# Kernel optimization log

Hardware: AMD Instinct MI355X
Metric: run time of the kernel (lower is better)

Reference implementation:

```python
import jax, jax.numpy as jnp
import numpy as np


def conv1x1(x, W, b):
    # x: [B,C,H,W], W: [O,C], b: [O]
    return jnp.einsum('bchw,oc->bohw', x, W) + b[None, :, None, None]


def setup_inputs() -> dict:
    key = jax.random.key(0)
    ks = jax.random.split(key, 16)
    B, C, H, W = 4, 256, 64, 64
    C4 = C // 4
    s = lambda fan_in: 1.0 / np.sqrt(fan_in)
    inp = {
        'last_frame': jax.random.normal(ks[0], (B, C, H, W), jnp.float32),
        'current_frame': jax.random.normal(ks[1], (B, C, H, W), jnp.float32),
        'future_frame': jax.random.normal(ks[2], (B, C, H, W), jnp.float32),
        'Wqk': jax.random.normal(ks[3], (C4, C), jnp.float32) * s(C),
        'bqk': jnp.zeros((C4,), jnp.float32),
        'Wkl': jax.random.normal(ks[4], (C4, C), jnp.float32) * s(C),
        'bkl': jnp.zeros((C4,), jnp.float32),
        'Wkf': jax.random.normal(ks[5], (C4, C), jnp.float32) * s(C),
        'bkf': jnp.zeros((C4,), jnp.float32),
        'Wv': jax.random.normal(ks[6], (C4, C), jnp.float32) * s(C),
        'bv': jnp.zeros((C4,), jnp.float32),
        'Wfire': jax.random.normal(ks[7], (C, C // 2), jnp.float32) * s(C // 2),
        'bfire': jnp.zeros((C,), jnp.float32),
        'bn_gamma': jnp.ones((C,), jnp.float32),
        'bn_beta': jnp.zeros((C,), jnp.float32),
        'bn_mean': jnp.zeros((C,), jnp.float32),
        'bn_var': jnp.ones((C,), jnp.float32),
    }
    return inp


def reference(last_frame, current_frame, future_frame,
              Wqk, bqk, Wkl, bkl, Wkf, bkf, Wv, bv,
              Wfire, bfire, bn_gamma, bn_beta, bn_mean, bn_var):
    B, C, H, W = current_frame.shape
    C4 = C // 4
    HW = H * W
    eps = 1e-5

    q = conv1x1(current_frame, Wqk, bqk).reshape(B, C4, HW)       # [B,C4,HW]
    kl = conv1x1(last_frame, Wkl, bkl).reshape(B, C4, HW)          # [B,C4,HW]
    kf = conv1x1(future_frame, Wkf, bkf).reshape(B, C4, HW)        # [B,C4,HW]
    v = conv1x1(current_frame, Wv, bv).reshape(B, C4, HW)          # [B,C4,HW]

    # affinity: [B, HW(query), HW(key)], softmax over key axis
    aff_l = jax.nn.softmax(jnp.einsum('bcq,bck->bqk', q, kl), axis=-1)
    aff_f = jax.nn.softmax(jnp.einsum('bcq,bck->bqk', q, kf), axis=-1)

    # out = V @ A^T : out[b,c,q] = sum_k v[b,c,k] * aff[b,q,k]
    out_l = jnp.einsum('bck,bqk->bcq', v, aff_l).reshape(B, C4, H, W)
    out_f = jnp.einsum('bck,bqk->bcq', v, aff_f).reshape(B, C4, H, W)

    fused = jnp.concatenate([out_l, out_f], axis=1)                 # [B,C/2,H,W]
    fired = conv1x1(fused, Wfire, bfire)                            # [B,C,H,W]
    # BatchNorm (inference form with running stats)
    inv = bn_gamma / jnp.sqrt(bn_var + eps)
    fired = fired * inv[None, :, None, None] + (bn_beta - bn_mean * inv)[None, :, None, None]
    return jax.nn.relu(current_frame + fired)
```

## Files before the change

### kernel.cpp

```cpp
#include <hip/hip_runtime.h>
#include <math.h>
#include <stdint.h>

#define HWN 4096
#define CIN 256
#define CQ 64
#define LOG2E 1.44269504f
#define C2OFF 56.0f

typedef __attribute__((ext_vector_type(8))) _Float16 f16x8;
typedef __attribute__((ext_vector_type(4))) _Float16 f16x4;
typedef __attribute__((ext_vector_type(8))) short    bf16x8;
typedef __attribute__((ext_vector_type(4))) short    bf16x4;
typedef __attribute__((ext_vector_type(4))) float    f32x4;

__device__ __forceinline__ short f2bf(float f) {
  union { float f; uint32_t u; } c; c.f = f;
  uint32_t r = (c.u + 0x7FFFu + ((c.u >> 16) & 1u)) >> 16;
  return (short)(uint16_t)r;
}

__device__ __forceinline__ void stage16(const void* g, void* l) {
  __builtin_amdgcn_global_load_lds(
      (const __attribute__((address_space(1))) uint32_t*)g,
      (__attribute__((address_space(3))) uint32_t*)l, 16, 0, 0);
}

__global__ __launch_bounds__(256) void prep_kernel(
    const float* __restrict__ Wqk, const float* __restrict__ Wkl,
    const float* __restrict__ Wkf, const float* __restrict__ Wv,
    const float* __restrict__ Wfire, const float* __restrict__ bfire,
    const float* __restrict__ gamma, const float* __restrict__ beta,
    const float* __restrict__ mean,  const float* __restrict__ var,
    _Float16* __restrict__ wqk_h, _Float16* __restrict__ wkl_h,
    _Float16* __restrict__ wkf_h, _Float16* __restrict__ wv_h,
    _Float16* __restrict__ wf_h, float* __restrict__ scale, float* __restrict__ shift) {
  int gid = blockIdx.x * 256 + threadIdx.x;
  if (gid < CQ * CIN) {
    wqk_h[gid] = (_Float16)(Wqk[gid] * LOG2E);
    wkl_h[gid] = (_Float16)Wkl[gid];
    wkf_h[gid] = (_Float16)Wkf[gid];
    wv_h[gid]  = (_Float16)Wv[gid];
  }
  if (gid < CIN * 128) wf_h[gid] = (_Float16)Wfire[gid];
  if (gid < CIN) {
    float inv = gamma[gid] / sqrtf(var[gid] + 1e-5f);
    scale[gid] = inv;
    shift[gid] = (bfire[gid] - mean[gid]) * inv + beta[gid];
  }
}

__global__ __launch_bounds__(256, 3) void proj_kernel(
    const float* __restrict__ cur, const float* __restrict__ last, const float* __restrict__ fut,
    const _Float16* __restrict__ wqk, const float* __restrict__ bqk,
    const _Float16* __restrict__ wkl, const float* __restrict__ bkl,
    const _Float16* __restrict__ wkf, const float* __restrict__ bkf,
    const _Float16* __restrict__ wv,  const float* __restrict__ bv,
    _Float16* __restrict__ q_out, _Float16* __restrict__ kl_out,
    _Float16* __restrict__ kf_out, short* __restrict__ v_out) {
  const int tid  = threadIdx.x;
  const int w    = tid >> 6;
  const int lane = tid & 63;
  const int quad = lane >> 4;
  const int l15  = lane & 15;
  const int pass = blockIdx.x >> 8;
  const int bb   = blockIdx.x & 255;
  const int b    = bb >> 6;
  const int hwt  = (bb & 63) << 6;
  const int hw   = hwt + w * 16 + l15;

  __shared__ __align__(16) _Float16 Tl[4][16][72];

  const float* X = (pass == 0) ? cur : ((pass == 1) ? last : fut);
  const float* xp = X + (size_t)b * CIN * HWN + hw;

  float xb[8][8];
#pragma unroll
  for (int c0 = 0; c0 < 8; ++c0)
#pragma unroll
    for (int j = 0; j < 8; ++j)
      xb[c0][j] = xp[(size_t)(c0 * 32 + quad * 8 + j) * HWN];

  if (pass == 0) {
    f32x4 aq[4] = {}; f32x4 av[4] = {};
#pragma unroll
    for (int k0 = 0; k0 < 8; ++k0) {
      f16x8 bh;
#pragma unroll
      for (int j = 0; j < 8; ++j) bh[j] = (_Float16)xb[k0][j];
#pragma unroll
      for (int mt = 0; mt < 4; ++mt) {
        f16x8 wa = *(const f16x8*)(wqk + (mt * 16 + l15) * CIN + k0 * 32 + quad * 8);
        aq[mt] = __builtin_amdgcn_mfma_f32_16x16x32_f16(wa, bh, aq[mt], 0, 0, 0);
        f16x8 wb = *(const f16x8*)(wv + (mt * 16 + l15) * CIN + k0 * 32 + quad * 8);
        av[mt] = __builtin_amdgcn_mfma_f32_16x16x32_f16(wb, bh, av[mt], 0, 0, 0);
      }
    }
#pragma unroll
    for (int mt = 0; mt < 4; ++mt)
#pragma unroll
      for (int r = 0; r < 4; ++r) {
        int oc = mt * 16 + quad * 4 + r;
        q_out[((size_t)b * CQ + oc) * HWN + hw] = (_Float16)(aq[mt][r] + bqk[oc] * LOG2E);
        v_out[((size_t)b * CQ + oc) * HWN + hw] = f2bf(av[mt][r] + bv[oc]);
      }
  } else {
    const _Float16* W = (pass == 1) ? wkl : wkf;
    const float* BI = (pass == 1) ? bkl : bkf;
    _Float16* OUT = (pass == 1) ? kl_out : kf_out;
    f32x4 a[4] = {};
#pragma unroll
    for (int k0 = 0; k0 < 8; ++k0) {
      f16x8 bh;
#pragma unroll
      for (int j = 0; j < 8; ++j) bh[j] = (_Float16)xb[k0][j];
#pragma unroll
      for (int mt = 0; mt < 4; ++mt) {
        f16x8 wa = *(const f16x8*)(W + (mt * 16 + l15) * CIN + k0 * 32 + quad * 8);
        a[mt] = __builtin_amdgcn_mfma_f32_16x16x32_f16(wa, bh, a[mt], 0, 0, 0);
      }
    }
#pragma unroll
    for (int mt = 0; mt < 4; ++mt) {
      f16x4 pw;
#pragma unroll
      for (int r = 0; r < 4; ++r)
        pw[r] = (_Float16)(a[mt][r] + BI[mt * 16 + quad * 4 + r]);
      *(f16x4*)&Tl[w][l15][mt * 16 + quad * 4] = pw;
    }
#pragma unroll
    for (int kk = 0; kk < 2; ++kk) {
      f16x8 row = *(const f16x8*)&Tl[w][l15][kk * 32 + quad * 8];
      *(f16x8*)(OUT + ((size_t)b * HWN + hw) * CQ + kk * 32 + quad * 8) = row;
    }
  }
}

__global__ __launch_bounds__(256, 2) void attn_kernel(
    const _Float16* __restrict__ qbuf, const _Float16* __restrict__ klbuf,
    const _Float16* __restrict__ kfbuf, const short* __restrict__ vbuf,
    _Float16* __restrict__ fused) {
  const int tid  = threadIdx.x;
  const int w    = tid >> 6;
  const int lane = tid & 63;
  const int quad = lane >> 4;
  const int l15  = lane & 15;
  const int bx   = blockIdx.x;
  const int pair = bx & 1;
  const int b    = (bx >> 1) & 3;
  const int qt   = (bx >> 3) << 6;

  const _Float16* K  = (pair ? kfbuf : klbuf) + (size_t)b * HWN * CQ;
  const short*    Vg = vbuf + (size_t)b * CQ * HWN;

  __shared__ __align__(16) _Float16 Kt[2][64][64];
  __shared__ __align__(16) short    Vt[2][64][64];
  __shared__ __align__(16) short    Pl[4][16][72];

  const int qbase = qt + w * 16;
  f16x8 qfrag[2];
#pragma unroll
  for (int kk = 0; kk < 2; ++kk)
#pragma unroll
    for (int j = 0; j < 8; ++j)
      qfrag[kk][j] = qbuf[(b * CQ + kk * 32 + quad * 8 + j) * HWN + qbase + l15];

  f32x4 Oacc[4] = {};
  float psum = 0.f;

  const int swz = (lane & 7) ^ ((lane >> 3) & 7);
  const int rswz = l15 & 7;

  auto stageK = [&](int buf, int t) {
#pragma unroll
    for (int r = 0; r < 2; ++r)
      stage16(K + (size_t)(t * 64 + w * 16 + r * 8 + (lane >> 3)) * CQ + swz * 8,
              &Kt[buf][w * 16 + r * 8][0]);
  };
  auto stageV = [&](int buf, int t) {
#pragma unroll
    for (int r = 0; r < 2; ++r)
      stage16(Vg + (size_t)(w * 16 + r * 8 + (lane >> 3)) * HWN + t * 64 + swz * 8,
              &Vt[buf][w * 16 + r * 8][0]);
  };

  auto body = [&](int buf) {
    f16x8 kf[4][2];
#pragma unroll
    for (int nt = 0; nt < 4; ++nt)
#pragma unroll
      for (int kk = 0; kk < 2; ++kk)
        kf[nt][kk] = *(const f16x8*)&Kt[buf][nt * 16 + l15][((kk * 4 + quad) ^ rswz) * 8];
    bf16x8 vf[4][2];
#pragma unroll
    for (int ct = 0; ct < 4; ++ct)
#pragma unroll
      for (int kk = 0; kk < 2; ++kk)
        vf[ct][kk] = *(const bf16x8*)&Vt[buf][ct * 16 + l15][((kk * 4 + quad) ^ rswz) * 8];
    f32x4 ST[4] = {};
#pragma unroll
    for (int nt = 0; nt < 4; ++nt)
#pragma unroll
      for (int kk = 0; kk < 2; ++kk)
        ST[nt] = __builtin_amdgcn_mfma_f32_16x16x32_f16(kf[nt][kk], qfrag[kk], ST[nt], 0, 0, 0);
#pragma unroll
    for (int nt = 0; nt < 4; ++nt) {
      bf16x4 pw;
#pragma unroll
      for (int r = 0; r < 4; ++r) {
        float p = __builtin_amdgcn_exp2f(ST[nt][r] - C2OFF);
        uint32_t u = __float_as_uint(p) & 0xffff0000u;
        psum += __uint_as_float(u);
        pw[r] = (short)(u >> 16);
      }
      *(bf16x4*)&Pl[w][l15][nt * 16 + quad * 4] = pw;
    }
#pragma unroll
    for (int kk = 0; kk < 2; ++kk) {
      bf16x8 pf = *(const bf16x8*)&Pl[w][l15][kk * 32 + quad * 8];
#pragma unroll
      for (int ct = 0; ct < 4; ++ct)
        Oacc[ct] = __builtin_amdgcn_mfma_f32_16x16x32_bf16(pf, vf[ct][kk], Oacc[ct], 0, 0, 0);
    }
  };

  stageK(0, 0); stageV(0, 0);
  __syncthreads();
#pragma unroll 1
  for (int tt = 0; tt < 64; tt += 2) {
    stageK(1, tt + 1); stageV(1, tt + 1);
    body(0);
    __syncthreads();
    if (tt + 2 < 64) { stageK(0, tt + 2); stageV(0, tt + 2); }
    body(1);
    __syncthreads();
  }

  psum += __shfl_xor(psum, 16);
  psum += __shfl_xor(psum, 32);

#pragma unroll
  for (int r = 0; r < 4; ++r) {
    float lt = __shfl(psum, quad * 4 + r);
    float invl = __builtin_amdgcn_rcpf(lt);
    int qi = qbase + quad * 4 + r;
#pragma unroll
    for (int ct = 0; ct < 4; ++ct)
      fused[((size_t)b * HWN + qi) * 128 + pair * 64 + ct * 16 + l15] =
          (_Float16)(Oacc[ct][r] * invl);
  }
}

__global__ __launch_bounds__(256) void fire_kernel(
    const _Float16* __restrict__ fused, const _Float16* __restrict__ wf,
    const float* __restrict__ scale, const float* __restrict__ shift,
    const float* __restrict__ cur, float* __restrict__ out) {
  const int tid  = threadIdx.x;
  const int w    = tid >> 6;
  const int lane = tid & 63;
  const int quad = lane >> 4;
  const int l15  = lane & 15;
  const int g    = blockIdx.x & 3;
  const int bb   = blockIdx.x >> 2;
  const int b    = bb >> 6;
  const int hwt  = (bb & 63) << 6;
  const int hwb  = hwt + w * 16;

  f16x8 bfr[4];
#pragma unroll
  for (int k0 = 0; k0 < 4; ++k0)
    bfr[k0] = *(const f16x8*)(fused + ((size_t)b * HWN + hwb + l15) * 128 + k0 * 32 + quad * 8);

  float curv[4][4];
#pragma unroll
  for (int mt = 0; mt < 4; ++mt)
#pragma unroll
    for (int r = 0; r < 4; ++r)
      curv[mt][r] = cur[((size_t)b * CIN + g * 64 + mt * 16 + quad * 4 + r) * HWN + hwb + l15];

  f32x4 acc[4] = {};
#pragma unroll
  for (int k0 = 0; k0 < 4; ++k0)
#pragma unroll
    for (int mt = 0; mt < 4; ++mt) {
      f16x8 af = *(const f16x8*)(wf + (g * 64 + mt * 16 + l15) * 128 + k0 * 32 + quad * 8);
      acc[mt] = __builtin_amdgcn_mfma_f32_16x16x32_f16(af, bfr[k0], acc[mt], 0, 0, 0);
    }

#pragma unroll
  for (int mt = 0; mt < 4; ++mt)
#pragma unroll
    for (int r = 0; r < 4; ++r) {
      int oc = g * 64 + mt * 16 + quad * 4 + r;
      size_t idx = ((size_t)b * CIN + oc) * HWN + hwb + l15;
      float y = curv[mt][r] + acc[mt][r] * scale[oc] + shift[oc];
      out[idx] = fmaxf(y, 0.f);
    }
}

extern "C" void kernel_launch(void* const* d_in, const int* in_sizes, int n_in,
                              void* d_out, int out_size, void* d_ws, size_t ws_size,
                              hipStream_t stream) {
  const float* last  = (const float*)d_in[0];
  const float* cur   = (const float*)d_in[1];
  const float* fut   = (const float*)d_in[2];
  const float* Wqk   = (const float*)d_in[3];
  const float* bqk   = (const float*)d_in[4];
  const float* Wkl   = (const float*)d_in[5];
  const float* bkl   = (const float*)d_in[6];
  const float* Wkf   = (const float*)d_in[7];
  const float* bkf   = (const float*)d_in[8];
  const float* Wv    = (const float*)d_in[9];
  const float* bv    = (const float*)d_in[10];
  const float* Wfire = (const float*)d_in[11];
  const float* bfire = (const float*)d_in[12];
  const float* gamma = (const float*)d_in[13];
  const float* beta  = (const float*)d_in[14];
  const float* mean  = (const float*)d_in[15];
  const float* var   = (const float*)d_in[16];

  char* ws = (char*)d_ws;
  _Float16* qb     = (_Float16*)(ws);
  _Float16* klb    = (_Float16*)(ws + (2u << 20));
  _Float16* kfb    = (_Float16*)(ws + (4u << 20));
  short*    vb     = (short*)   (ws + (6u << 20));
  _Float16* fusedb = (_Float16*)(ws + (8u << 20));
  char* wsm = ws + (12u << 20);
  _Float16* wqk_h = (_Float16*)(wsm);
  _Float16* wkl_h = (_Float16*)(wsm + (32u << 10));
  _Float16* wkf_h = (_Float16*)(wsm + (64u << 10));
  _Float16* wv_h  = (_Float16*)(wsm + (96u << 10));
  _Float16* wf_h  = (_Float16*)(wsm + (128u << 10));
  float*    scale = (float*)   (wsm + (192u << 10));
  float*    shift = (float*)   (wsm + (193u << 10));
  float*    out   = (float*)d_out;

  prep_kernel<<<128, 256, 0, stream>>>(Wqk, Wkl, Wkf, Wv, Wfire, bfire,
                                       gamma, beta, mean, var,
                                       wqk_h, wkl_h, wkf_h, wv_h, wf_h, scale, shift);
  proj_kernel<<<768, 256, 0, stream>>>(cur, last, fut, wqk_h, bqk, wkl_h, bkl,
                                       wkf_h, bkf, wv_h, bv, qb, klb, kfb, vb);
  attn_kernel<<<512, 256, 0, stream>>>(qb, klb, kfb, vb, fusedb);
  fire_kernel<<<1024, 256, 0, stream>>>(fusedb, wf_h, scale, shift, cur, out);
}
```

Before: 203.9 us.

## Split key range across wave pairs, read V from global, remap blocks per XCD

The attention kernel now splits its waves into two key halves. Each wave handles 32 queries instead of 16, which reuses each staged K tile across two query groups. The two halves' partial outputs and row sums are combined through shared memory at the end. V fragments are now loaded directly from global memory instead of being staged in LDS, only K is double-buffered, block indices are remapped so each XCD gets contiguous work, and MFMA sections get raised wave priority. This aims to cut LDS traffic and per-query K staging and to improve L2 locality, at the cost of more registers, uncoalesced direct V loads and an extra reduction step.

```diff
diff --git a/kernel.cpp b/kernel.cpp
--- a/kernel.cpp
+++ b/kernel.cpp
@@ -145,109 +145,149 @@
   const int lane = tid & 63;
   const int quad = lane >> 4;
   const int l15  = lane & 15;
-  const int bx   = blockIdx.x;
-  const int pair = bx & 1;
-  const int b    = (bx >> 1) & 3;
-  const int qt   = (bx >> 3) << 6;
+
+  const int xcd  = blockIdx.x & 7;
+  const int L    = xcd * 64 + (blockIdx.x >> 3);
+  const int qt   = (L & 63) << 6;
+  const int pair = (L >> 6) & 1;
+  const int b    = L >> 7;
+
+  const int kh = w >> 1;
+  const int wq = w & 1;
 
   const _Float16* K  = (pair ? kfbuf : klbuf) + (size_t)b * HWN * CQ;
   const short*    Vg = vbuf + (size_t)b * CQ * HWN;
 
-  __shared__ __align__(16) _Float16 Kt[2][64][64];
-  __shared__ __align__(16) short    Vt[2][64][64];
-  __shared__ __align__(16) short    Pl[4][16][72];
-
-  const int qbase = qt + w * 16;
-  f16x8 qfrag[2];
-#pragma unroll
-  for (int kk = 0; kk < 2; ++kk)
-#pragma unroll
-    for (int j = 0; j < 8; ++j)
-      qfrag[kk][j] = qbuf[(b * CQ + kk * 32 + quad * 8 + j) * HWN + qbase + l15];
-
-  f32x4 Oacc[4] = {};
-  float psum = 0.f;
-
-  const int swz = (lane & 7) ^ ((lane >> 3) & 7);
+  __shared__ __align__(16) _Float16 Kt[2][2][64][64];
+  __shared__ __align__(16) short    Pl[4][32][72];
+
+  const int qbase = qt + wq * 32;
+  f16x8 qfrag[2][2];
+#pragma unroll
+  for (int qg = 0; qg < 2; ++qg)
+#pragma unroll
+    for (int kk = 0; kk < 2; ++kk)
+#pragma unroll
+      for (int j = 0; j < 8; ++j)
+        qfrag[qg][kk][j] = qbuf[(b * CQ + kk * 32 + quad * 8 + j) * HWN +
+                                qbase + qg * 16 + l15];
+
+  f32x4 Oacc[2][4] = {};
+  float psum[2] = {0.f, 0.f};
+
+  const int swz  = (lane & 7) ^ ((lane >> 3) & 7);
   const int rswz = l15 & 7;
 
+  const _Float16* ksrc =
+      K + ((size_t)(kh * 32) * 64 + wq * 32 + (lane >> 3)) * CQ + swz * 8;
+  const short* vsrc = Vg + (size_t)l15 * HWN + kh * 2048 + quad * 8;
+
   auto stageK = [&](int buf, int t) {
 #pragma unroll
-    for (int r = 0; r < 2; ++r)
-      stage16(K + (size_t)(t * 64 + w * 16 + r * 8 + (lane >> 3)) * CQ + swz * 8,
-              &Kt[buf][w * 16 + r * 8][0]);
+    for (int r = 0; r < 4; ++r)
+      stage16(ksrc + ((size_t)t * 64 + r * 8) * CQ,
+              &Kt[buf][kh][wq * 32 + r * 8][0]);
   };
-  auto stageV = [&](int buf, int t) {
-#pragma unroll
-    for (int r = 0; r < 2; ++r)
-      stage16(Vg + (size_t)(w * 16 + r * 8 + (lane >> 3)) * HWN + t * 64 + swz * 8,
-              &Vt[buf][w * 16 + r * 8][0]);
+
+  auto body = [&](int buf, int t) {
+    bf16x8 vf[4][2];
+#pragma unroll
+    for (int ct = 0; ct < 4; ++ct)
+#pragma unroll
+      for (int kk = 0; kk < 2; ++kk)
+        vf[ct][kk] = *(const bf16x8*)(vsrc + (size_t)ct * 16 * HWN + t * 64 + kk * 32);
+    f16x8 kf[4][2];
+#pragma unroll
+    for (int nt = 0; nt < 4; ++nt)
+#pragma unroll
+      for (int kk = 0; kk < 2; ++kk)
+        kf[nt][kk] = *(const f16x8*)&Kt[buf][kh][nt * 16 + l15][((kk * 4 + quad) ^ rswz) * 8];
+#pragma unroll
+    for (int qg = 0; qg < 2; ++qg) {
+      f32x4 ST[4] = {};
+      __builtin_amdgcn_s_setprio(1);
+#pragma unroll
+      for (int nt = 0; nt < 4; ++nt)
+#pragma unroll
+        for (int kk = 0; kk < 2; ++kk)
+          ST[nt] = __builtin_amdgcn_mfma_f32_16x16x32_f16(kf[nt][kk], qfrag[qg][kk],
+                                                          ST[nt], 0, 0, 0);
+      __builtin_amdgcn_s_setprio(0);
+#pragma unroll
+      for (int nt = 0; nt < 4; ++nt) {
+        bf16x4 pw;
+#pragma unroll
+        for (int r = 0; r < 4; ++r) {
+          float p = __builtin_amdgcn_exp2f(ST[nt][r] - C2OFF);
+          uint32_t u = __float_as_uint(p) & 0xffff0000u;
+          psum[qg] += __uint_as_float(u);
+          pw[r] = (short)(u >> 16);
+        }
+        *(bf16x4*)&Pl[w][qg * 16 + l15][nt * 16 + quad * 4] = pw;
+      }
+#pragma unroll
+      for (int kk = 0; kk < 2; ++kk) {
+        bf16x8 pf = *(const bf16x8*)&Pl[w][qg * 16 + l15][kk * 32 + quad * 8];
+        __builtin_amdgcn_s_setprio(1);
+#pragma unroll
+        for (int ct = 0; ct < 4; ++ct)
+          Oacc[qg][ct] = __builtin_amdgcn_mfma_f32_16x16x32_bf16(pf, vf[ct][kk],
+                                                                 Oacc[qg][ct], 0, 0, 0);
+        __builtin_amdgcn_s_setprio(0);
+      }
+    }
   };
 
-  auto body = [&](int buf) {
-    f16x8 kf[4][2];
-#pragma unroll
-    for (int nt = 0; nt < 4; ++nt)
-#pragma unroll
-      for (int kk = 0; kk < 2; ++kk)
-        kf[nt][kk] = *(const f16x8*)&Kt[buf][nt * 16 + l15][((kk * 4 + quad) ^ rswz) * 8];
-    bf16x8 vf[4][2];
-#pragma unroll
-    for (int ct = 0; ct < 4; ++ct)
-#pragma unroll
-      for (int kk = 0; kk < 2; ++kk)
-        vf[ct][kk] = *(const bf16x8*)&Vt[buf][ct * 16 + l15][((kk * 4 + quad) ^ rswz) * 8];
-    f32x4 ST[4] = {};
-#pragma unroll
-    for (int nt = 0; nt < 4; ++nt)
-#pragma unroll
-      for (int kk = 0; kk < 2; ++kk)
-        ST[nt] = __builtin_amdgcn_mfma_f32_16x16x32_f16(kf[nt][kk], qfrag[kk], ST[nt], 0, 0, 0);
-#pragma unroll
-    for (int nt = 0; nt < 4; ++nt) {
-      bf16x4 pw;
-#pragma unroll
-      for (int r = 0; r < 4; ++r) {
-        float p = __builtin_amdgcn_exp2f(ST[nt][r] - C2OFF);
-        uint32_t u = __float_as_uint(p) & 0xffff0000u;
-        psum += __uint_as_float(u);
-        pw[r] = (short)(u >> 16);
-      }
-      *(bf16x4*)&Pl[w][l15][nt * 16 + quad * 4] = pw;
-    }
-#pragma unroll
-    for (int kk = 0; kk < 2; ++kk) {
-      bf16x8 pf = *(const bf16x8*)&Pl[w][l15][kk * 32 + quad * 8];
-#pragma unroll
-      for (int ct = 0; ct < 4; ++ct)
-        Oacc[ct] = __builtin_amdgcn_mfma_f32_16x16x32_bf16(pf, vf[ct][kk], Oacc[ct], 0, 0, 0);
-    }
-  };
-
-  stageK(0, 0); stageV(0, 0);
+  stageK(0, 0);
   __syncthreads();
 #pragma unroll 1
-  for (int tt = 0; tt < 64; tt += 2) {
-    stageK(1, tt + 1); stageV(1, tt + 1);
-    body(0);
+  for (int tt = 0; tt < 32; tt += 2) {
+    stageK(1, tt + 1);
+    body(0, tt);
     __syncthreads();
-    if (tt + 2 < 64) { stageK(0, tt + 2); stageV(0, tt + 2); }
-    body(1);
+    if (tt + 2 < 32) stageK(0, tt + 2);
+    body(1, tt + 1);
     __syncthreads();
   }
 
-  psum += __shfl_xor(psum, 16);
-  psum += __shfl_xor(psum, 32);
-
-#pragma unroll
-  for (int r = 0; r < 4; ++r) {
-    float lt = __shfl(psum, quad * 4 + r);
-    float invl = __builtin_amdgcn_rcpf(lt);
-    int qi = qbase + quad * 4 + r;
-#pragma unroll
-    for (int ct = 0; ct < 4; ++ct)
-      fused[((size_t)b * HWN + qi) * 128 + pair * 64 + ct * 16 + l15] =
-          (_Float16)(Oacc[ct][r] * invl);
+#pragma unroll
+  for (int qg = 0; qg < 2; ++qg) {
+    psum[qg] += __shfl_xor(psum[qg], 16);
+    psum[qg] += __shfl_xor(psum[qg], 32);
+  }
+
+  float* sc = (float*)&Kt[0][0][0][0];
+  float* sp = sc + 4096;
+  if (kh) {
+#pragma unroll
+    for (int qg = 0; qg < 2; ++qg) {
+#pragma unroll
+      for (int ct = 0; ct < 4; ++ct)
+        *(f32x4*)&sc[((((wq * 2 + qg) * 4) + ct) << 8) + lane * 4] = Oacc[qg][ct];
+      sp[(wq * 2 + qg) * 64 + lane] = psum[qg];
+    }
+  }
+  __syncthreads();
+  if (!kh) {
+#pragma unroll
+    for (int qg = 0; qg < 2; ++qg) {
+      psum[qg] += sp[(wq * 2 + qg) * 64 + lane];
+#pragma unroll
+      for (int ct = 0; ct < 4; ++ct) {
+        f32x4 o2 = *(const f32x4*)&sc[((((wq * 2 + qg) * 4) + ct) << 8) + lane * 4];
+        Oacc[qg][ct] += o2;
+      }
+#pragma unroll
+      for (int r = 0; r < 4; ++r) {
+        float lt = __shfl(psum[qg], quad * 4 + r);
+        float invl = __builtin_amdgcn_rcpf(lt);
+        int qi = qbase + qg * 16 + quad * 4 + r;
+#pragma unroll
+        for (int ct = 0; ct < 4; ++ct)
+          fused[((size_t)b * HWN + qi) * 128 + pair * 64 + ct * 16 + l15] =
+              (_Float16)(Oacc[qg][ct][r] * invl);
+      }
+    }
   }
 }
 
```

After: 214.4 us. 5.2% more time.
